# Kernel tuning notes

Hardware: AMD Instinct MI355X
Metric: run time of the kernel (lower is better)

Reference implementation:

```python
import jax, jax.numpy as jnp
import numpy as np

NEG_BIG = -9e15
ALPHA = 0.2  # LeakyReLU negative slope


def setup_inputs() -> dict:
    key = jax.random.key(0)
    k1, k2, k3, k4 = jax.random.split(key, 4)
    B, N, Fin, Fout = 4, 2048, 128, 128
    h = jax.random.normal(k1, (B, N, Fin), dtype=jnp.float32)
    adj = jax.random.randint(k2, (N, N), 0, 2, dtype=jnp.int32)
    W = jax.random.normal(k3, (Fin, Fout), dtype=jnp.float32) * 0.1
    a = jax.random.normal(k4, (2 * Fout, 1), dtype=jnp.float32) * 0.1
    return {"h": h, "adj": adj, "W": W, "a": a}


def reference(h, adj, W, a):
    # Wh: [B, N, Fout]
    Wh = jnp.einsum('bnf,fo->bno', h, W)
    Fout = W.shape[1]
    a1 = a[:Fout, 0]   # attends to source i
    a2 = a[Fout:, 0]   # attends to target j
    # Decomposed form of leakyrelu(cat([Wh_i, Wh_j]) @ a):
    # e_ij = leakyrelu(a1.Wh_i + a2.Wh_j)  -> [B, N, N]
    f1 = Wh @ a1  # [B, N]
    f2 = Wh @ a2  # [B, N]
    e = jax.nn.leaky_relu(f1[:, :, None] + f2[:, None, :], negative_slope=ALPHA)
    attention = jnp.where(adj[None, :, :] > 0, e, jnp.float32(NEG_BIG))
    attention = jax.nn.softmax(attention, axis=2)
    # dropout is identity in eval mode
    h_prime = jnp.einsum('bij,bjo->bio', attention, Wh)
    return h_prime
```

## Files before the change

kernel.cpp:

```cpp
#include <hip/hip_runtime.h>

#define BB 4
#define NN 2048
#define FF 128
#define ALPHA 0.2f
#define SHIFT_C 16.0f

typedef short bf16x8 __attribute__((ext_vector_type(8)));
typedef short bf16x4 __attribute__((ext_vector_type(4)));
typedef float f32x4 __attribute__((ext_vector_type(4)));
typedef unsigned u32;

__device__ inline short f2bf(float f) {
    union { float f; unsigned u; } v; v.f = f;
    unsigned r = (v.u + 0x7FFFu + ((v.u >> 16) & 1u)) >> 16;
    return (short)r;
}
__device__ inline float bf2f(short s) {
    union { float f; unsigned u; } v;
    v.u = ((unsigned)(unsigned short)s) << 16;
    return v.f;
}

__device__ inline void cp16(const void* g, void* l) {
    __builtin_amdgcn_global_load_lds(
        (const __attribute__((address_space(1))) u32*)g,
        (__attribute__((address_space(3))) u32*)l, 16, 0, 0);
}

__global__ __launch_bounds__(256) void k_wh(const float* __restrict__ h,
                                            const float* __restrict__ W,
                                            const float* __restrict__ a,
                                            const int* __restrict__ adj,
                                            short* __restrict__ WhHiT,
                                            short* __restrict__ WhLoT,
                                            float* __restrict__ f1,
                                            float* __restrict__ f2,
                                            u32* __restrict__ adjp) {
    __shared__ float Wa[2 * FF];
    __shared__ float hs[16 * 128];
    int tid = threadIdx.x;
    int r0 = blockIdx.x * 16;

    {
        int fin = tid & 127;
        const float* av = (tid < 128) ? a : (a + FF);
        const float* wr = W + (size_t)fin * FF;
        float s = 0.f;
        for (int o = 0; o < FF; o += 4) {
            float4 wv = *(const float4*)(wr + o);
            float4 avv = *(const float4*)(av + o);
            s += wv.x * avv.x + wv.y * avv.y + wv.z * avv.z + wv.w * avv.w;
        }
        Wa[(tid < 128 ? 0 : FF) + fin] = s;
    }
    {
        const float4* src = (const float4*)(h + (size_t)r0 * FF);
        float4* dst = (float4*)hs;
        dst[tid] = src[tid];
        dst[256 + tid] = src[256 + tid];
    }
    {
        int w = tid >> 6, lane = tid & 63;
        int row = blockIdx.x * 4 + w;
        const int* ar = adj + (size_t)row * NN;
        for (int it = 0; it < 32; ++it) {
            int v = ar[it * 64 + lane];
            unsigned long long mask = __ballot(v > 0);
            if (lane == 0) adjp[row * 64 + it * 2] = (u32)mask;
            if (lane == 1) adjp[row * 64 + it * 2 + 1] = (u32)(mask >> 32);
        }
    }
    __syncthreads();

    {
        int w = tid >> 6, lane = tid & 63;
        float wa1_0 = Wa[lane], wa1_1 = Wa[lane + 64];
        float wa2_0 = Wa[FF + lane], wa2_1 = Wa[FF + lane + 64];
        for (int rr = 0; rr < 4; ++rr) {
            int rloc = w * 4 + rr;
            int row = r0 + rloc;
            float x0 = hs[rloc * FF + lane], x1 = hs[rloc * FF + lane + 64];
            float s1 = x0 * wa1_0 + x1 * wa1_1;
            float s2 = x0 * wa2_0 + x1 * wa2_1;
#pragma unroll
            for (int m = 32; m >= 1; m >>= 1) {
                s1 += __shfl_xor(s1, m, 64);
                s2 += __shfl_xor(s2, m, 64);
            }
            if (lane == 0) { f1[row] = s1; f2[row] = s2; }
        }
    }

    int f4 = (tid & 31) * 4;
    int rg = tid >> 5;
    float acc[2][4];
#pragma unroll
    for (int rr = 0; rr < 2; ++rr)
#pragma unroll
        for (int cc = 0; cc < 4; ++cc) acc[rr][cc] = 0.f;

    for (int k0 = 0; k0 < FF; k0 += 4) {
        float4 wv[4];
#pragma unroll
        for (int kk = 0; kk < 4; ++kk)
            wv[kk] = *(const float4*)(W + (size_t)(k0 + kk) * FF + f4);
        float4 hv[2];
#pragma unroll
        for (int rr = 0; rr < 2; ++rr)
            hv[rr] = *(const float4*)(hs + (rg * 2 + rr) * FF + k0);
#pragma unroll
        for (int rr = 0; rr < 2; ++rr) {
            float hk[4] = {hv[rr].x, hv[rr].y, hv[rr].z, hv[rr].w};
#pragma unroll
            for (int kk = 0; kk < 4; ++kk) {
                acc[rr][0] += hk[kk] * wv[kk].x;
                acc[rr][1] += hk[kk] * wv[kk].y;
                acc[rr][2] += hk[kk] * wv[kk].z;
                acc[rr][3] += hk[kk] * wv[kk].w;
            }
        }
    }
    int rloc = r0 + rg * 2;
    int b = rloc >> 11;
    int j = rloc & (NN - 1);
#pragma unroll
    for (int cc = 0; cc < 4; ++cc) {
        float v0 = acc[0][cc], v1 = acc[1][cc];
        short h0 = f2bf(v0), h1 = f2bf(v1);
        short l0 = f2bf(v0 - bf2f(h0)), l1 = f2bf(v1 - bf2f(h1));
        size_t off = (size_t)(b * FF + f4 + cc) * NN + j;
        *(short2*)(WhHiT + off) = make_short2(h0, h1);
        *(short2*)(WhLoT + off) = make_short2(l0, l1);
    }
}

__global__ __launch_bounds__(512, 2) void k_attn(const short* __restrict__ WhHiT,
                                                 const short* __restrict__ WhLoT,
                                                 const u32* __restrict__ adjp,
                                                 const float* __restrict__ f1,
                                                 const float* __restrict__ f2,
                                                 float* __restrict__ out) {
    __shared__ __align__(16) char lds[39040];
    char* B0 = lds;
    char* A0 = lds + 32768;
    float* row_ps = (float*)(lds + 37888);
    float* row_inv = (float*)(lds + 38912);

    int tid = threadIdx.x;
    int w = tid >> 6, lane = tid & 63;
    int blk = blockIdx.x;
    int b = blk >> 6;
    int i0 = (blk & 63) * 32;

    int r_a = lane & 15, kg = lane >> 4;
    int mi = w >> 2, ni = w & 3;

    int rb = tid & 31;
    int jp = tid >> 5;
    float f1i = f1[b * NN + i0 + rb];
    const u32* aprow = adjp + (size_t)(i0 + rb) * 64;
    const float* f2b = f2 + b * NN;
    int aoff = (rb >> 4) * 1280 + (rb & 15) * 80 + jp * 4;

    int fo_s = w * 16 + (lane >> 2);
    int oc_s = lane & 3;
    const short* gH = WhHiT + (size_t)(b * FF + fo_s) * NN + oc_s * 8;
    const short* gL = WhLoT + (size_t)(b * FF + fo_s) * NN + oc_s * 8;
    int bH = w * 1024;
    int bL = 8192 + w * 1024;

    f32x4 acc0 = {0.f, 0.f, 0.f, 0.f}, acc1 = {0.f, 0.f, 0.f, 0.f};
    float sp = 0.f;

    cp16(gH, B0 + bH);
    cp16(gL, B0 + bL);
    {
        float2 q = *(const float2*)(f2b + jp * 2);
        u32 mw = aprow[0];
        float x0 = f1i + q.x, x1 = f1i + q.y;
        x0 = fmaxf(x0, ALPHA * x0);
        x1 = fmaxf(x1, ALPHA * x1);
        float p0 = __expf(x0 - SHIFT_C) * (float)((mw >> (jp * 2)) & 1u);
        float p1 = __expf(x1 - SHIFT_C) * (float)((mw >> (jp * 2 + 1)) & 1u);
        sp += p0 + p1;
        union { float f; u32 u; } u0, u1; u0.f = p0; u1.f = p1;
        *(u32*)(A0 + aoff) = ((u0.u + 0x8000u) >> 16) | (((u1.u + 0x8000u) >> 16) << 16);
    }
    float2 pf2 = *(const float2*)(f2b + 32 + jp * 2);
    u32 pmw = aprow[1];
    __syncthreads();

    for (int s = 0; s < 64; ++s) {
        {
            int jn = ((s + 1) & 63) * 32;
            char* wb = B0 + ((s + 1) & 1) * 16384;
            cp16(gH + jn, wb + bH);
            cp16(gL + jn, wb + bL);
        }
        {
            char* wa = A0 + ((s + 1) & 1) * 2560;
            float x0 = f1i + pf2.x, x1 = f1i + pf2.y;
            x0 = fmaxf(x0, ALPHA * x0);
            x1 = fmaxf(x1, ALPHA * x1);
            float p0 = __expf(x0 - SHIFT_C) * (float)((pmw >> (jp * 2)) & 1u);
            float p1 = __expf(x1 - SHIFT_C) * (float)((pmw >> (jp * 2 + 1)) & 1u);
            if (s < 63) sp += p0 + p1;
            union { float f; u32 u; } u0, u1; u0.f = p0; u1.f = p1;
            *(u32*)(wa + aoff) = ((u0.u + 0x8000u) >> 16) | (((u1.u + 0x8000u) >> 16) << 16);
        }
        {
            int sn = (s + 2) & 63;
            pf2 = *(const float2*)(f2b + sn * 32 + jp * 2);
            pmw = aprow[sn];
        }
        {
            char* rbuf = B0 + (s & 1) * 16384;
            char* abuf = A0 + (s & 1) * 2560;
            bf16x8 af = *(const bf16x8*)(abuf + mi * 1280 + r_a * 80 + kg * 16);
            int n0 = ni * 2;
            const char* p0 = rbuf + ((n0 * 16 + r_a) * 64 + kg * 16);
            const char* p1 = rbuf + (((n0 + 1) * 16 + r_a) * 64 + kg * 16);
            bf16x8 b0h = *(const bf16x8*)p0;
            bf16x8 b0l = *(const bf16x8*)(p0 + 8192);
            bf16x8 b1h = *(const bf16x8*)p1;
            bf16x8 b1l = *(const bf16x8*)(p1 + 8192);
            acc0 = __builtin_amdgcn_mfma_f32_16x16x32_bf16(af, b0h, acc0, 0, 0, 0);
            acc0 = __builtin_amdgcn_mfma_f32_16x16x32_bf16(af, b0l, acc0, 0, 0, 0);
            acc1 = __builtin_amdgcn_mfma_f32_16x16x32_bf16(af, b1h, acc1, 0, 0, 0);
            acc1 = __builtin_amdgcn_mfma_f32_16x16x32_bf16(af, b1l, acc1, 0, 0, 0);
        }
        __syncthreads();
    }

    sp += __shfl_xor(sp, 32, 64);
    if (lane < 32) row_ps[w * 32 + lane] = sp;
    __syncthreads();
    if (tid < 32) {
        float t = 0.f;
#pragma unroll
        for (int ww = 0; ww < 8; ++ww) t += row_ps[ww * 32 + tid];
        row_inv[tid] = 1.0f / t;
    }
    __syncthreads();

    float* ob = out + ((size_t)b * NN + i0 + mi * 16) * FF + ni * 32;
#pragma unroll
    for (int q = 0; q < 4; ++q) {
        int rr = kg * 4 + q;
        float inv = row_inv[mi * 16 + rr];
        ob[(size_t)rr * FF + r_a] = acc0[q] * inv;
        ob[(size_t)rr * FF + 16 + r_a] = acc1[q] * inv;
    }
}

extern "C" void kernel_launch(void* const* d_in, const int* in_sizes, int n_in,
                              void* d_out, int out_size, void* d_ws, size_t ws_size,
                              hipStream_t stream) {
    const float* h   = (const float*)d_in[0];
    const int*   adj = (const int*)d_in[1];
    const float* W   = (const float*)d_in[2];
    const float* a   = (const float*)d_in[3];
    float* out = (float*)d_out;

    short* WhHiT = (short*)d_ws;
    short* WhLoT = WhHiT + (size_t)BB * FF * NN;
    float* f1 = (float*)(WhLoT + (size_t)BB * FF * NN);
    float* f2 = f1 + (size_t)BB * NN;
    u32* adjp = (u32*)(f2 + (size_t)BB * NN);

    k_wh<<<(BB * NN) / 16, 256, 0, stream>>>(h, W, a, adj, WhHiT, WhLoT, f1, f2, adjp);
    k_attn<<<BB * (NN / 32), 512, 0, stream>>>(WhHiT, WhLoT, adjp, f1, f2, out);
}
```

Before: 149.8 us.

## Double attention block waves, triple-buffer Wh tiles, and pad transposed Wh rows

```diff
diff --git a/kernel.cpp b/kernel.cpp
--- a/kernel.cpp
+++ b/kernel.cpp
@@ -3,11 +3,11 @@
 #define BB 4
 #define NN 2048
 #define FF 128
+#define NP 2176
 #define ALPHA 0.2f
 #define SHIFT_C 16.0f
 
 typedef short bf16x8 __attribute__((ext_vector_type(8)));
-typedef short bf16x4 __attribute__((ext_vector_type(4)));
 typedef float f32x4 __attribute__((ext_vector_type(4)));
 typedef unsigned u32;
 
@@ -129,23 +129,23 @@
         float v0 = acc[0][cc], v1 = acc[1][cc];
         short h0 = f2bf(v0), h1 = f2bf(v1);
         short l0 = f2bf(v0 - bf2f(h0)), l1 = f2bf(v1 - bf2f(h1));
-        size_t off = (size_t)(b * FF + f4 + cc) * NN + j;
+        size_t off = (size_t)(b * FF + f4 + cc) * NP + j;
         *(short2*)(WhHiT + off) = make_short2(h0, h1);
         *(short2*)(WhLoT + off) = make_short2(l0, l1);
     }
 }
 
-__global__ __launch_bounds__(512, 2) void k_attn(const short* __restrict__ WhHiT,
-                                                 const short* __restrict__ WhLoT,
-                                                 const u32* __restrict__ adjp,
-                                                 const float* __restrict__ f1,
-                                                 const float* __restrict__ f2,
-                                                 float* __restrict__ out) {
-    __shared__ __align__(16) char lds[39040];
-    char* B0 = lds;
-    char* A0 = lds + 32768;
-    float* row_ps = (float*)(lds + 37888);
-    float* row_inv = (float*)(lds + 38912);
+__global__ __launch_bounds__(1024, 4) void k_attn(const short* __restrict__ WhHiT,
+                                                  const short* __restrict__ WhLoT,
+                                                  const u32* __restrict__ adjp,
+                                                  const float* __restrict__ f1,
+                                                  const float* __restrict__ f2,
+                                                  float* __restrict__ out) {
+    __shared__ __align__(16) char lds[55424];
+    char* Bbuf = lds;
+    char* A0 = lds + 49152;
+    float* row_ps = (float*)(lds + 54272);
+    float* row_inv = (float*)(lds + 55296);
 
     int tid = threadIdx.x;
     int w = tid >> 6, lane = tid & 63;
@@ -154,28 +154,30 @@
     int i0 = (blk & 63) * 32;
 
     int r_a = lane & 15, kg = lane >> 4;
-    int mi = w >> 2, ni = w & 3;
+    int mi = w >> 3, ni = w & 7;
 
     int rb = tid & 31;
-    int jp = tid >> 5;
-    float f1i = f1[b * NN + i0 + rb];
+    int jp = (tid >> 5) & 15;
+    bool abuild = tid < 512;
+    float f1i = abuild ? f1[b * NN + i0 + rb] : 0.f;
     const u32* aprow = adjp + (size_t)(i0 + rb) * 64;
     const float* f2b = f2 + b * NN;
     int aoff = (rb >> 4) * 1280 + (rb & 15) * 80 + jp * 4;
 
-    int fo_s = w * 16 + (lane >> 2);
+    int hw = w & 7;
+    int isLo = w >> 3;
+    int fo_s = hw * 16 + (lane >> 2);
     int oc_s = lane & 3;
-    const short* gH = WhHiT + (size_t)(b * FF + fo_s) * NN + oc_s * 8;
-    const short* gL = WhLoT + (size_t)(b * FF + fo_s) * NN + oc_s * 8;
-    int bH = w * 1024;
-    int bL = 8192 + w * 1024;
-
-    f32x4 acc0 = {0.f, 0.f, 0.f, 0.f}, acc1 = {0.f, 0.f, 0.f, 0.f};
+    const short* gB = (isLo ? WhLoT : WhHiT) + (size_t)(b * FF + fo_s) * NP + oc_s * 8;
+    int bB = isLo * 8192 + hw * 1024;
+
+    f32x4 acc = {0.f, 0.f, 0.f, 0.f};
     float sp = 0.f;
 
-    cp16(gH, B0 + bH);
-    cp16(gL, B0 + bL);
-    {
+    cp16(gB, Bbuf + bB);
+    float2 pf2 = {0.f, 0.f};
+    u32 pmw = 0;
+    if (abuild) {
         float2 q = *(const float2*)(f2b + jp * 2);
         u32 mw = aprow[0];
         float x0 = f1i + q.x, x1 = f1i + q.y;
@@ -186,19 +188,18 @@
         sp += p0 + p1;
         union { float f; u32 u; } u0, u1; u0.f = p0; u1.f = p1;
         *(u32*)(A0 + aoff) = ((u0.u + 0x8000u) >> 16) | (((u1.u + 0x8000u) >> 16) << 16);
-    }
-    float2 pf2 = *(const float2*)(f2b + 32 + jp * 2);
-    u32 pmw = aprow[1];
-    __syncthreads();
-
+        pf2 = *(const float2*)(f2b + 32 + jp * 2);
+        pmw = aprow[1];
+    }
+    __syncthreads();
+
+    int cur = 0, nxt = 1;
     for (int s = 0; s < 64; ++s) {
         {
             int jn = ((s + 1) & 63) * 32;
-            char* wb = B0 + ((s + 1) & 1) * 16384;
-            cp16(gH + jn, wb + bH);
-            cp16(gL + jn, wb + bL);
-        }
-        {
+            cp16(gB + jn, Bbuf + nxt * 16384 + bB);
+        }
+        if (abuild) {
             char* wa = A0 + ((s + 1) & 1) * 2560;
             float x0 = f1i + pf2.x, x1 = f1i + pf2.y;
             x0 = fmaxf(x0, ALPHA * x0);
@@ -208,33 +209,27 @@
             if (s < 63) sp += p0 + p1;
             union { float f; u32 u; } u0, u1; u0.f = p0; u1.f = p1;
             *(u32*)(wa + aoff) = ((u0.u + 0x8000u) >> 16) | (((u1.u + 0x8000u) >> 16) << 16);
-        }
-        {
             int sn = (s + 2) & 63;
             pf2 = *(const float2*)(f2b + sn * 32 + jp * 2);
             pmw = aprow[sn];
         }
         {
-            char* rbuf = B0 + (s & 1) * 16384;
+            char* rbuf = Bbuf + cur * 16384;
             char* abuf = A0 + (s & 1) * 2560;
             bf16x8 af = *(const bf16x8*)(abuf + mi * 1280 + r_a * 80 + kg * 16);
-            int n0 = ni * 2;
-            const char* p0 = rbuf + ((n0 * 16 + r_a) * 64 + kg * 16);
-            const char* p1 = rbuf + (((n0 + 1) * 16 + r_a) * 64 + kg * 16);
-            bf16x8 b0h = *(const bf16x8*)p0;
-            bf16x8 b0l = *(const bf16x8*)(p0 + 8192);
-            bf16x8 b1h = *(const bf16x8*)p1;
-            bf16x8 b1l = *(const bf16x8*)(p1 + 8192);
-            acc0 = __builtin_amdgcn_mfma_f32_16x16x32_bf16(af, b0h, acc0, 0, 0, 0);
-            acc0 = __builtin_amdgcn_mfma_f32_16x16x32_bf16(af, b0l, acc0, 0, 0, 0);
-            acc1 = __builtin_amdgcn_mfma_f32_16x16x32_bf16(af, b1h, acc1, 0, 0, 0);
-            acc1 = __builtin_amdgcn_mfma_f32_16x16x32_bf16(af, b1l, acc1, 0, 0, 0);
+            const char* p = rbuf + ((ni * 16 + r_a) * 64 + kg * 16);
+            bf16x8 bh = *(const bf16x8*)p;
+            bf16x8 bl = *(const bf16x8*)(p + 8192);
+            acc = __builtin_amdgcn_mfma_f32_16x16x32_bf16(af, bh, acc, 0, 0, 0);
+            acc = __builtin_amdgcn_mfma_f32_16x16x32_bf16(af, bl, acc, 0, 0, 0);
         }
         __syncthreads();
+        cur = nxt;
+        nxt = (nxt == 2) ? 0 : nxt + 1;
     }
 
     sp += __shfl_xor(sp, 32, 64);
-    if (lane < 32) row_ps[w * 32 + lane] = sp;
+    if (w < 8 && lane < 32) row_ps[w * 32 + lane] = sp;
     __syncthreads();
     if (tid < 32) {
         float t = 0.f;
@@ -244,13 +239,11 @@
     }
     __syncthreads();
 
-    float* ob = out + ((size_t)b * NN + i0 + mi * 16) * FF + ni * 32;
+    float* ob = out + ((size_t)b * NN + i0 + mi * 16) * FF + ni * 16;
 #pragma unroll
     for (int q = 0; q < 4; ++q) {
         int rr = kg * 4 + q;
-        float inv = row_inv[mi * 16 + rr];
-        ob[(size_t)rr * FF + r_a] = acc0[q] * inv;
-        ob[(size_t)rr * FF + 16 + r_a] = acc1[q] * inv;
+        ob[(size_t)rr * FF + r_a] = acc[q] * row_inv[mi * 16 + rr];
     }
 }
 
@@ -264,11 +257,11 @@
     float* out = (float*)d_out;
 
     short* WhHiT = (short*)d_ws;
-    short* WhLoT = WhHiT + (size_t)BB * FF * NN;
-    float* f1 = (float*)(WhLoT + (size_t)BB * FF * NN);
+    short* WhLoT = WhHiT + (size_t)BB * FF * NP;
+    float* f1 = (float*)(WhLoT + (size_t)BB * FF * NP);
     float* f2 = f1 + (size_t)BB * NN;
     u32* adjp = (u32*)(f2 + (size_t)BB * NN);
 
     k_wh<<<(BB * NN) / 16, 256, 0, stream>>>(h, W, a, adj, WhHiT, WhLoT, f1, f2, adjp);
-    k_attn<<<BB * (NN / 32), 512, 0, stream>>>(WhHiT, WhLoT, adjp, f1, f2, out);
-}
+    k_attn<<<BB * (NN / 32), 1024, 0, stream>>>(WhHiT, WhLoT, adjp, f1, f2, out);
+}
```

New measurement: 149.1 us. About the same (-0.5%).
